# Kernel optimization log

Measured on AMD Instinct MI355X. Metric: run time of the kernel, lower is better.

The kernel has to match this reference:

```python
import jax, jax.numpy as jnp
import numpy as np

ALPHA, GAMMA = 0.25, 2.0
COST_CLASS, COST_BBOX, COST_GIOU = 2.0, 5.0, 2.0
EPS = 1e-8


def box_cxcywh_to_xyxy(b):
    cx, cy, w, h = b[..., 0], b[..., 1], b[..., 2], b[..., 3]
    return jnp.stack([cx - 0.5 * w, cy - 0.5 * h, cx + 0.5 * w, cy + 0.5 * h], axis=-1)


def generalized_box_iou(boxes1, boxes2):
    # boxes1: [N,4] xyxy, boxes2: [M,4] xyxy -> [N,M] GIoU
    area1 = (boxes1[:, 2] - boxes1[:, 0]) * (boxes1[:, 3] - boxes1[:, 1])
    area2 = (boxes2[:, 2] - boxes2[:, 0]) * (boxes2[:, 3] - boxes2[:, 1])
    lt = jnp.maximum(boxes1[:, None, :2], boxes2[None, :, :2])   # [N,M,2]
    rb = jnp.minimum(boxes1[:, None, 2:], boxes2[None, :, 2:])   # [N,M,2]
    wh = jnp.clip(rb - lt, 0.0)
    inter = wh[..., 0] * wh[..., 1]
    union = area1[:, None] + area2[None, :] - inter
    iou = inter / union
    # smallest enclosing box
    lt_c = jnp.minimum(boxes1[:, None, :2], boxes2[None, :, :2])
    rb_c = jnp.maximum(boxes1[:, None, 2:], boxes2[None, :, 2:])
    wh_c = jnp.clip(rb_c - lt_c, 0.0)
    area_c = wh_c[..., 0] * wh_c[..., 1]
    return iou - (area_c - union) / area_c


def setup_inputs() -> dict:
    key = jax.random.key(0)
    k1, k2, k3, k4 = jax.random.split(key, 4)
    BS, NQ, NC, NT = 16, 900, 91, 960
    pred_logits = jax.random.normal(k1, (BS, NQ, NC), dtype=jnp.float32)
    pred_boxes = jax.random.uniform(k2, (BS, NQ, 4), dtype=jnp.float32)
    tgt_ids = jax.random.randint(k3, (NT,), 0, NC, dtype=jnp.int64)
    tgt_bbox = jax.random.uniform(k4, (NT, 4), dtype=jnp.float32)
    return {"pred_logits": pred_logits, "pred_boxes": pred_boxes,
            "tgt_ids": tgt_ids, "tgt_bbox": tgt_bbox}


def reference(pred_logits, pred_boxes, tgt_ids, tgt_bbox):
    bs, nq, _ = pred_logits.shape
    out_prob = jax.nn.sigmoid(pred_logits.reshape(bs * nq, -1))      # [BN, C]
    out_bbox = pred_boxes.reshape(bs * nq, 4)                         # [BN, 4]
    # focal-style classification cost, gathered at target class ids
    neg_cost = (1.0 - ALPHA) * out_prob ** GAMMA * (-jnp.log(1.0 - out_prob + EPS))
    pos_cost = ALPHA * (1.0 - out_prob) ** GAMMA * (-jnp.log(out_prob + EPS))
    cost_class = pos_cost[:, tgt_ids] - neg_cost[:, tgt_ids]          # [BN, NT]
    # pairwise L1 distance between boxes (cxcywh space), like torch.cdist(p=1)
    cost_bbox = jnp.sum(jnp.abs(out_bbox[:, None, :] - tgt_bbox[None, :, :]), axis=-1)
    cost_giou = -generalized_box_iou(box_cxcywh_to_xyxy(out_bbox),
                                     box_cxcywh_to_xyxy(tgt_bbox))    # [BN, NT]
    C = COST_BBOX * cost_bbox + COST_CLASS * cost_class + COST_GIOU * cost_giou
    return C.reshape(bs, nq, -1)
```

## Files before the change

kernel.cpp:

```cpp
#include <hip/hip_runtime.h>
#include <math.h>


#define ALPHA_F   0.25f
#define COST_CLS  2.0f
#define COST_BBOX 5.0f
#define COST_GIOU 2.0f
#define EPS_F     1e-8f

constexpr int THREADS = 256;

__device__ __forceinline__ float focal_entry(float x) {
    const float p  = 1.0f / (1.0f + __expf(-x));
    const float om = 1.0f - p;
    const float neg = (1.0f - ALPHA_F) * p * p * (-__logf(om + EPS_F));
    const float pos = ALPHA_F * om * om        * (-__logf(p  + EPS_F));
    return COST_CLS * (pos - neg) + COST_GIOU;
}

template<int NC, int NT>
__global__ __launch_bounds__(THREADS) void matcher_kernel_s(
    const float* __restrict__ logits,
    const float* __restrict__ boxes,
    const int*   __restrict__ tids,
    const float* __restrict__ tboxes,
    float*       __restrict__ out)
{
    constexpr int ROWS = 2;
    constexpr int JPT  = 4;
    constexpr int NJT  = NT / JPT;
    constexpr int NTAB = ROWS * NC;
    constexpr int CSTR = 3;

    __shared__ float s_cls[NC * CSTR];

    const int tid  = threadIdx.x;
    const int row0 = blockIdx.x * ROWS;
    const bool active = tid < NJT;

    float x = 0.0f;
    if (tid < NTAB)
        x = logits[(size_t)row0 * NC + tid];

    float4 tb[JPT];
    int ic[JPT] = {0, 0, 0, 0};
    if (active) {
        #pragma unroll
        for (int k = 0; k < JPT; ++k) {
            tb[k] = reinterpret_cast<const float4*>(tboxes)[tid + k * NJT];
            ic[k] = tids[tid + k * NJT];
        }
    } else {
        #pragma unroll
        for (int k = 0; k < JPT; ++k) tb[k] = make_float4(0.f, 0.f, 0.f, 0.f);
    }

    if (tid < NTAB) {
        const int r = (tid >= NC) ? 1 : 0;
        const int c = tid - (r ? NC : 0);
        s_cls[c * CSTR + r] = focal_entry(x);
    }
    __syncthreads();

    if (!active) return;

    float cc0[JPT], cc1[JPT];
    #pragma unroll
    for (int k = 0; k < JPT; ++k) {
        const float* cp = s_cls + ic[k] * CSTR;
        cc0[k] = cp[0];
        cc1[k] = cp[1];
    }

    float* __restrict__ obase = out + (size_t)row0 * NT + tid;
    #pragma unroll
    for (int r = 0; r < ROWS; ++r) {
        const float4 pb = reinterpret_cast<const float4*>(boxes)[row0 + r];
        const float px0 = pb.x - 0.5f * pb.z, py0 = pb.y - 0.5f * pb.w;
        const float px1 = pb.x + 0.5f * pb.z, py1 = pb.y + 0.5f * pb.w;
        const float parea = pb.z * pb.w;

        #pragma unroll
        for (int k = 0; k < JPT; ++k) {
            const float4 t = tb[k];
            const float hw = 0.5f * t.z, hh = 0.5f * t.w;
            const float tx0 = t.x - hw, tx1 = t.x + hw;
            const float ty0 = t.y - hh, ty1 = t.y + hh;
            const float tarea = t.z * t.w;
            const float l1 = (fabsf(pb.x - t.x) + fabsf(pb.y - t.y))
                           + (fabsf(pb.z - t.z) + fabsf(pb.w - t.w));
            const float iwr = fminf(px1, tx1) - fmaxf(px0, tx0);
            const float ihr = fminf(py1, ty1) - fmaxf(py0, ty0);
            const float inter = fmaxf(iwr, 0.0f) * fmaxf(ihr, 0.0f);
            const float uni = (parea + tarea) - inter;
            const float cw = (pb.z + t.z) - iwr;
            const float ch = (pb.w + t.w) - ihr;
            const float carea = cw * ch;
            const float num  = fmaf(inter, carea, uni * uni);
            const float rcpd = __builtin_amdgcn_rcpf(uni * carea);
            const float ctab = (r == 0) ? cc0[k] : cc1[k];
            const float base = fmaf(COST_BBOX, l1, ctab);
            const float v = fmaf(-2.0f * num, rcpd, base);
            obase[(size_t)r * NT + k * NJT] = v;
        }
    }
}

constexpr int GROWS = 8;
__global__ __launch_bounds__(THREADS) void matcher_kernel_g(
    const float* __restrict__ logits, const float* __restrict__ boxes,
    const int* __restrict__ tids, const float* __restrict__ tboxes,
    float* __restrict__ out, int BN, int NC, int NT)
{
    extern __shared__ float s_cls_g[];
    const int tid  = threadIdx.x;
    const int row0 = blockIdx.x * GROWS;
    const int nrows = (BN - row0 < GROWS) ? (BN - row0) : GROWS;

    for (int t = tid; t < nrows * NC; t += THREADS) {
        const int r = t / NC, c = t - r * NC;
        const float x = logits[(size_t)(row0 + r) * NC + c];
        const float p  = 1.0f / (1.0f + expf(-x));
        const float om = 1.0f - p;
        const float neg = (1.0f - ALPHA_F) * p * p * (-logf(om + EPS_F));
        const float pos = ALPHA_F * om * om        * (-logf(p + EPS_F));
        s_cls_g[r * NC + c] = pos - neg;
    }
    __syncthreads();

    for (int r = 0; r < nrows; ++r) {
        const int row = row0 + r;
        const float4 pb = reinterpret_cast<const float4*>(boxes)[row];
        const float px0 = pb.x - 0.5f * pb.z, py0 = pb.y - 0.5f * pb.w;
        const float px1 = pb.x + 0.5f * pb.z, py1 = pb.y + 0.5f * pb.w;
        const float parea = pb.z * pb.w;
        for (int j = tid; j < NT; j += THREADS) {
            const float4 b = reinterpret_cast<const float4*>(tboxes)[j];
            const float bx0 = b.x - 0.5f * b.z, by0 = b.y - 0.5f * b.w;
            const float bx1 = b.x + 0.5f * b.z, by1 = b.y + 0.5f * b.w;
            const float l1 = fabsf(pb.x - b.x) + fabsf(pb.y - b.y)
                           + fabsf(pb.z - b.z) + fabsf(pb.w - b.w);
            const float iw = fmaxf(fminf(px1, bx1) - fmaxf(px0, bx0), 0.0f);
            const float ih = fmaxf(fminf(py1, by1) - fmaxf(py0, by0), 0.0f);
            const float inter = iw * ih;
            const float uni = parea + b.z * b.w - inter;
            const float iou = inter / uni;
            const float cw = fmaxf(px1, bx1) - fminf(px0, bx0);
            const float ch = fmaxf(py1, by1) - fminf(py0, by0);
            const float carea = cw * ch;
            const float giou = iou - (carea - uni) / carea;
            const float ccls = s_cls_g[r * NC + tids[j]];
            out[(size_t)row * NT + j] = COST_BBOX * l1 + COST_CLS * ccls - COST_GIOU * giou;
        }
        __syncthreads();
    }
}

extern "C" void kernel_launch(void* const* d_in, const int* in_sizes, int n_in,
                              void* d_out, int out_size, void* d_ws, size_t ws_size,
                              hipStream_t stream) {
    const float* logits = (const float*)d_in[0];
    const float* boxes  = (const float*)d_in[1];
    const int*   tids   = (const int*)d_in[2];
    const float* tboxes = (const float*)d_in[3];
    float* out = (float*)d_out;

    const int BN = in_sizes[1] / 4;
    const int NC = in_sizes[0] / BN;
    const int NT = in_sizes[2];

    if (NC == 91 && NT == 960 && BN % 2 == 0) {
        matcher_kernel_s<91, 960><<<BN / 2, THREADS, 0, stream>>>(
            logits, boxes, tids, tboxes, out);
    } else {
        const int grid = (BN + GROWS - 1) / GROWS;
        const size_t shmem = (size_t)GROWS * NC * sizeof(float);
        matcher_kernel_g<<<grid, THREADS, shmem, stream>>>(
            logits, boxes, tids, tboxes, out, BN, NC, NT);
    }
}
```

Baseline: 22.41 us.

## Use 192-thread blocks, softplus focal math, and nontemporal output stores

```diff
diff --git a/kernel.cpp b/kernel.cpp
--- a/kernel.cpp
+++ b/kernel.cpp
@@ -8,13 +8,15 @@
 #define COST_GIOU 2.0f
 #define EPS_F     1e-8f
 
-constexpr int THREADS = 256;
+constexpr int THREADS = 192;
 
 __device__ __forceinline__ float focal_entry(float x) {
-    const float p  = 1.0f / (1.0f + __expf(-x));
+    const float ex = __expf(x);
+    const float p  = ex / (1.0f + ex);
+    const float sp = __logf(1.0f + ex);
     const float om = 1.0f - p;
-    const float neg = (1.0f - ALPHA_F) * p * p * (-__logf(om + EPS_F));
-    const float pos = ALPHA_F * om * om        * (-__logf(p  + EPS_F));
+    const float pos = ALPHA_F * om * om * (sp - x);
+    const float neg = (1.0f - ALPHA_F) * p * p * sp;
     return COST_CLS * (pos - neg) + COST_GIOU;
 }
 
@@ -27,8 +29,7 @@
     float*       __restrict__ out)
 {
     constexpr int ROWS = 2;
-    constexpr int JPT  = 4;
-    constexpr int NJT  = NT / JPT;
+    constexpr int JPT  = NT / THREADS;
     constexpr int NTAB = ROWS * NC;
     constexpr int CSTR = 3;
 
@@ -36,23 +37,17 @@
 
     const int tid  = threadIdx.x;
     const int row0 = blockIdx.x * ROWS;
-    const bool active = tid < NJT;
 
     float x = 0.0f;
     if (tid < NTAB)
         x = logits[(size_t)row0 * NC + tid];
 
     float4 tb[JPT];
-    int ic[JPT] = {0, 0, 0, 0};
-    if (active) {
-        #pragma unroll
-        for (int k = 0; k < JPT; ++k) {
-            tb[k] = reinterpret_cast<const float4*>(tboxes)[tid + k * NJT];
-            ic[k] = tids[tid + k * NJT];
-        }
-    } else {
-        #pragma unroll
-        for (int k = 0; k < JPT; ++k) tb[k] = make_float4(0.f, 0.f, 0.f, 0.f);
+    int ic[JPT];
+    #pragma unroll
+    for (int k = 0; k < JPT; ++k) {
+        tb[k] = reinterpret_cast<const float4*>(tboxes)[tid + k * THREADS];
+        ic[k] = tids[tid + k * THREADS];
     }
 
     if (tid < NTAB) {
@@ -61,8 +56,6 @@
         s_cls[c * CSTR + r] = focal_entry(x);
     }
     __syncthreads();
-
-    if (!active) return;
 
     float cc0[JPT], cc1[JPT];
     #pragma unroll
@@ -101,13 +94,14 @@
             const float ctab = (r == 0) ? cc0[k] : cc1[k];
             const float base = fmaf(COST_BBOX, l1, ctab);
             const float v = fmaf(-2.0f * num, rcpd, base);
-            obase[(size_t)r * NT + k * NJT] = v;
+            __builtin_nontemporal_store(v, obase + (size_t)r * NT + k * THREADS);
         }
     }
 }
 
+constexpr int GTHREADS = 256;
 constexpr int GROWS = 8;
-__global__ __launch_bounds__(THREADS) void matcher_kernel_g(
+__global__ __launch_bounds__(GTHREADS) void matcher_kernel_g(
     const float* __restrict__ logits, const float* __restrict__ boxes,
     const int* __restrict__ tids, const float* __restrict__ tboxes,
     float* __restrict__ out, int BN, int NC, int NT)
@@ -117,7 +111,7 @@
     const int row0 = blockIdx.x * GROWS;
     const int nrows = (BN - row0 < GROWS) ? (BN - row0) : GROWS;
 
-    for (int t = tid; t < nrows * NC; t += THREADS) {
+    for (int t = tid; t < nrows * NC; t += GTHREADS) {
         const int r = t / NC, c = t - r * NC;
         const float x = logits[(size_t)(row0 + r) * NC + c];
         const float p  = 1.0f / (1.0f + expf(-x));
@@ -134,7 +128,7 @@
         const float px0 = pb.x - 0.5f * pb.z, py0 = pb.y - 0.5f * pb.w;
         const float px1 = pb.x + 0.5f * pb.z, py1 = pb.y + 0.5f * pb.w;
         const float parea = pb.z * pb.w;
-        for (int j = tid; j < NT; j += THREADS) {
+        for (int j = tid; j < NT; j += GTHREADS) {
             const float4 b = reinterpret_cast<const float4*>(tboxes)[j];
             const float bx0 = b.x - 0.5f * b.z, by0 = b.y - 0.5f * b.w;
             const float bx1 = b.x + 0.5f * b.z, by1 = b.y + 0.5f * b.w;
@@ -175,7 +169,7 @@
     } else {
         const int grid = (BN + GROWS - 1) / GROWS;
         const size_t shmem = (size_t)GROWS * NC * sizeof(float);
-        matcher_kernel_g<<<grid, THREADS, shmem, stream>>>(
+        matcher_kernel_g<<<grid, GTHREADS, shmem, stream>>>(
             logits, boxes, tids, tboxes, out, BN, NC, NT);
     }
 }
```

Measured after the change: 19.68 us (median of 2 runs). -12.2%, faster.
